# Kernel tuning notes

Hardware: AMD Instinct MI355X
Metric: run time of the kernel (lower is better)

Reference implementation:

```python
import jax, jax.numpy as jnp
import numpy as np

N = 8192        # num nodes == input_dim (attn is [N,N], indexed by edge endpoints)
E = 262144      # num edges (nnz of sparse G), avg degree 32
OD = 64         # output_dim


def setup_inputs() -> dict:
    key = jax.random.key(0)
    k_x, k_r, k_c, k_v, k_a, k_w = jax.random.split(key, 6)
    x = jax.random.normal(k_x, (N, N), dtype=jnp.float32)
    row = jax.random.randint(k_r, (E,), 0, N)
    col = jax.random.randint(k_c, (E,), 0, N)
    values = jax.random.uniform(k_v, (E,), dtype=jnp.float32)
    attn = jax.random.uniform(k_a, (N, N), dtype=jnp.float32)  # init uniform(0,1) per reset_parameters
    stdv = 1.0 / np.sqrt(OD)
    weight = jax.random.uniform(k_w, (N, OD), dtype=jnp.float32, minval=-stdv, maxval=stdv)
    return {"x": x, "attn": attn, "weight": weight, "values": values, "row": row, "col": col}


def reference(x, attn, weight, values, row, col):
    # x = x @ W : [N, OD]
    y = x @ weight
    # sparse_dense_mul: scale each edge's value by attn[row, col] (irregular gather)
    ev = values * attn[row, col]                      # [E]
    # torch.sparse.mm(G, y): out[i] = sum_{e: row[e]==i} ev[e] * y[col[e]]
    out = jax.ops.segment_sum(ev[:, None] * y[col], row, num_segments=x.shape[0])
    return (out, jnp.linalg.norm(attn))
```

## Files before the change

kernel.cpp:

```cpp
#include <hip/hip_runtime.h>
#include <hip/hip_bf16.h>

#define N 8192
#define OD 64
#define E_EDGES 262144

#define BM 64
#define BK 64
#define KSPLIT 16
#define KS_PER_SPLIT (N / KSPLIT)
#define NTILES (KS_PER_SPLIT / BK)
#define NORM_BLOCKS 2048
#define SCAT_BLOCKS 8192

typedef __attribute__((ext_vector_type(8))) short bf16x8;
typedef __attribute__((ext_vector_type(4))) float f32x4;

__device__ __forceinline__ unsigned short f2bf(float f) {
    union { float f; unsigned u; } v; v.f = f;
    unsigned r = (v.u + 0x7fffu + ((v.u >> 16) & 1u)) >> 16;
    return (unsigned short)r;
}

__device__ __forceinline__ void gload16(const void* g, void* l) {
    __builtin_amdgcn_global_load_lds(
        (const __attribute__((address_space(1))) unsigned int*)g,
        (__attribute__((address_space(3))) unsigned int*)l, 16, 0, 0);
}

__global__ __launch_bounds__(256) void prep_kernel(const float* __restrict__ attn,
                                                   const float* __restrict__ w,
                                                   unsigned short* __restrict__ wt,
                                                   float4* __restrict__ y4,
                                                   float4* __restrict__ out4,
                                                   float* __restrict__ part) {
    const int bid = blockIdx.x, t = threadIdx.x;

    if (t < 128) {
        int zi = bid * 128 + t;
        float4 z{0.f, 0.f, 0.f, 0.f};
        if (zi < 131072) y4[zi] = z;
        else out4[zi - 131072] = z;
    }

    if (bid < 128) {
        __shared__ unsigned short lds[64][80];
        const int kb = bid * 64;
        #pragma unroll
        for (int p = 0; p < 4; ++p) {
            int idx = p * 1024 + t * 4;
            int r = idx >> 6, c = idx & 63;
            float4 v = *(const float4*)(&w[(size_t)(kb + r) * OD + c]);
            lds[c + 0][r] = f2bf(v.x);
            lds[c + 1][r] = f2bf(v.y);
            lds[c + 2][r] = f2bf(v.z);
            lds[c + 3][r] = f2bf(v.w);
        }
        __syncthreads();
        const int colx = t >> 2, j0 = (t & 3) * 16;
        #pragma unroll
        for (int u = 0; u < 2; ++u) {
            *(bf16x8*)(wt + (size_t)colx * N + kb + j0 + u * 8) =
                *(const bf16x8*)(&lds[colx][j0 + u * 8]);
        }
    }

    const float4* a4 = (const float4*)attn;
    const int total = (N * (long)N) / 4;
    float s = 0.f;
    for (long i = (long)bid * 256 + t; i < total; i += (long)NORM_BLOCKS * 256) {
        float4 v = a4[i];
        s += v.x * v.x + v.y * v.y + v.z * v.z + v.w * v.w;
    }
    for (int off = 32; off > 0; off >>= 1) s += __shfl_down(s, off, 64);
    __shared__ float wpart[4];
    int wid = t >> 6;
    if ((t & 63) == 0) wpart[wid] = s;
    __syncthreads();
    if (t == 0) part[bid] = wpart[0] + wpart[1] + wpart[2] + wpart[3];
}

__global__ __launch_bounds__(256) void gemm_kernel(const float* __restrict__ x,
                                                   const unsigned short* __restrict__ wt,
                                                   float* __restrict__ y) {
    __shared__ float xs[2][BM * BK];
    __shared__ unsigned short bs[2][BM * BK];

    const int t = threadIdx.x;
    const int wv = t >> 6, lane = t & 63;
    const int lrow = lane & 15, g = lane >> 4;
    const int sw = lrow & 7;
    const int row0 = blockIdx.x * BM;
    const int k0 = blockIdx.y * KS_PER_SPLIT;

    const int xrow_b = t >> 4, xchunk = t & 15;
    const int brow_b = t >> 3, bchunk = t & 7;

    f32x4 acc[4] = {f32x4{0,0,0,0}, f32x4{0,0,0,0}, f32x4{0,0,0,0}, f32x4{0,0,0,0}};

    #define STAGE(buf, tile)                                                          \
        {                                                                             \
            const int kk = k0 + (tile) * BK;                                          \
            _Pragma("unroll")                                                         \
            for (int j = 0; j < 4; ++j) {                                             \
                int r = j * 16 + xrow_b;                                              \
                gload16(&x[(size_t)(row0 + r) * N + kk + ((xchunk ^ (r & 7)) << 2)],  \
                        &xs[buf][j * 1024 + t * 4]);                                  \
            }                                                                         \
            _Pragma("unroll")                                                         \
            for (int j = 0; j < 2; ++j) {                                             \
                int r = j * 32 + brow_b;                                              \
                gload16(&wt[(size_t)r * N + kk + ((bchunk ^ (r & 7)) << 3)],          \
                        &bs[buf][j * 2048 + t * 8]);                                  \
            }                                                                         \
        }

    STAGE(0, 0);
    asm volatile("s_waitcnt vmcnt(0)" ::: "memory");
    __syncthreads();

    int cur = 0;
    for (int tile = 0; tile < NTILES; ++tile) {
        if (tile + 1 < NTILES) STAGE(cur ^ 1, tile + 1);
        const int ar = wv * 16 + lrow;
        #pragma unroll
        for (int ks = 0; ks < 2; ++ks) {
            const int c0 = ks * 8 + g * 2;
            float4 lo = *(const float4*)&xs[cur][ar * 64 + ((c0 ^ sw) << 2)];
            float4 hi = *(const float4*)&xs[cur][ar * 64 + (((c0 + 1) ^ sw) << 2)];
            bf16x8 a;
            a[0] = f2bf(lo.x); a[1] = f2bf(lo.y); a[2] = f2bf(lo.z); a[3] = f2bf(lo.w);
            a[4] = f2bf(hi.x); a[5] = f2bf(hi.y); a[6] = f2bf(hi.z); a[7] = f2bf(hi.w);
            #pragma unroll
            for (int cf = 0; cf < 4; ++cf) {
                const int rb = cf * 16 + lrow;
                bf16x8 b = *(const bf16x8*)&bs[cur][rb * 64 + (((ks * 4 + g) ^ sw) << 3)];
                acc[cf] = __builtin_amdgcn_mfma_f32_16x16x32_bf16(a, b, acc[cf], 0, 0, 0);
            }
        }
        asm volatile("s_waitcnt vmcnt(0)" ::: "memory");
        __syncthreads();
        cur ^= 1;
    }

    float* yp = y + ((size_t)row0 + wv * 16 + g * 4) * OD;
    #pragma unroll
    for (int cf = 0; cf < 4; ++cf) {
        #pragma unroll
        for (int i = 0; i < 4; ++i)
            atomicAdd(&yp[i * OD + cf * 16 + lrow], acc[cf][i]);
    }
    #undef STAGE
}

__global__ __launch_bounds__(256) void scatter_kernel(const float* __restrict__ values,
                                                      const float* __restrict__ attn,
                                                      const int* __restrict__ row,
                                                      const int* __restrict__ col,
                                                      const float* __restrict__ y,
                                                      float* __restrict__ out,
                                                      const float* __restrict__ part,
                                                      float* __restrict__ out_norm) {
    if (blockIdx.x == SCAT_BLOCKS) {
        float s = 0.f;
        #pragma unroll
        for (int k = 0; k < NORM_BLOCKS / 256; ++k) s += part[k * 256 + threadIdx.x];
        for (int off = 32; off > 0; off >>= 1) s += __shfl_down(s, off, 64);
        __shared__ float wp[4];
        int wid = threadIdx.x >> 6;
        if ((threadIdx.x & 63) == 0) wp[wid] = s;
        __syncthreads();
        if (threadIdx.x == 0) *out_norm = sqrtf(wp[0] + wp[1] + wp[2] + wp[3]);
        return;
    }
    const int lane = threadIdx.x & 63;
    int e = blockIdx.x * 4 + (threadIdx.x >> 6);
    #pragma unroll
    for (int it = 0; it < E_EDGES / (SCAT_BLOCKS * 4); ++it, e += SCAT_BLOCKS * 4) {
        const int r = row[e];
        const int c = col[e];
        const float ev = values[e] * attn[(size_t)r * N + c];
        atomicAdd(&out[r * OD + lane], ev * y[c * OD + lane]);
    }
}

extern "C" void kernel_launch(void* const* d_in, const int* in_sizes, int n_in,
                              void* d_out, int out_size, void* d_ws, size_t ws_size,
                              hipStream_t stream) {
    const float* x      = (const float*)d_in[0];
    const float* attn   = (const float*)d_in[1];
    const float* weight = (const float*)d_in[2];
    const float* values = (const float*)d_in[3];
    const int*   row    = (const int*)d_in[4];
    const int*   col    = (const int*)d_in[5];
    float* out = (float*)d_out;

    char* wsb = (char*)d_ws;
    float*          part = (float*)wsb;
    unsigned short* wt   = (unsigned short*)(wsb + (1u << 20));
    float*          y    = (float*)(wsb + (2u << 20));

    prep_kernel<<<NORM_BLOCKS, 256, 0, stream>>>(attn, weight, wt, (float4*)y,
                                                 (float4*)out, part);
    gemm_kernel<<<dim3(N / BM, KSPLIT), 256, 0, stream>>>(x, wt, y);
    scatter_kernel<<<SCAT_BLOCKS + 1, 256, 0, stream>>>(values, attn, row, col, y, out,
                                                        part, out + (size_t)N * OD);
}
```

Before: 182.2 us.

## Move attn norm reduction into scatter kernel and batch edge loads

```diff
diff --git a/kernel.cpp b/kernel.cpp
--- a/kernel.cpp
+++ b/kernel.cpp
@@ -10,8 +10,8 @@
 #define KSPLIT 16
 #define KS_PER_SPLIT (N / KSPLIT)
 #define NTILES (KS_PER_SPLIT / BK)
-#define NORM_BLOCKS 2048
 #define SCAT_BLOCKS 8192
+#define EDGE_ITERS (E_EDGES / (SCAT_BLOCKS * 4))
 
 typedef __attribute__((ext_vector_type(8))) short bf16x8;
 typedef __attribute__((ext_vector_type(4))) float f32x4;
@@ -28,56 +28,37 @@
         (__attribute__((address_space(3))) unsigned int*)l, 16, 0, 0);
 }
 
-__global__ __launch_bounds__(256) void prep_kernel(const float* __restrict__ attn,
-                                                   const float* __restrict__ w,
+__global__ __launch_bounds__(256) void prep_kernel(const float* __restrict__ w,
                                                    unsigned short* __restrict__ wt,
                                                    float4* __restrict__ y4,
-                                                   float4* __restrict__ out4,
-                                                   float* __restrict__ part) {
+                                                   float4* __restrict__ out4) {
     const int bid = blockIdx.x, t = threadIdx.x;
-
-    if (t < 128) {
-        int zi = bid * 128 + t;
-        float4 z{0.f, 0.f, 0.f, 0.f};
-        if (zi < 131072) y4[zi] = z;
-        else out4[zi - 131072] = z;
-    }
-
-    if (bid < 128) {
-        __shared__ unsigned short lds[64][80];
-        const int kb = bid * 64;
-        #pragma unroll
-        for (int p = 0; p < 4; ++p) {
-            int idx = p * 1024 + t * 4;
-            int r = idx >> 6, c = idx & 63;
-            float4 v = *(const float4*)(&w[(size_t)(kb + r) * OD + c]);
-            lds[c + 0][r] = f2bf(v.x);
-            lds[c + 1][r] = f2bf(v.y);
-            lds[c + 2][r] = f2bf(v.z);
-            lds[c + 3][r] = f2bf(v.w);
-        }
-        __syncthreads();
-        const int colx = t >> 2, j0 = (t & 3) * 16;
-        #pragma unroll
-        for (int u = 0; u < 2; ++u) {
-            *(bf16x8*)(wt + (size_t)colx * N + kb + j0 + u * 8) =
-                *(const bf16x8*)(&lds[colx][j0 + u * 8]);
-        }
-    }
-
-    const float4* a4 = (const float4*)attn;
-    const int total = (N * (long)N) / 4;
-    float s = 0.f;
-    for (long i = (long)bid * 256 + t; i < total; i += (long)NORM_BLOCKS * 256) {
-        float4 v = a4[i];
-        s += v.x * v.x + v.y * v.y + v.z * v.z + v.w * v.w;
-    }
-    for (int off = 32; off > 0; off >>= 1) s += __shfl_down(s, off, 64);
-    __shared__ float wpart[4];
-    int wid = t >> 6;
-    if ((t & 63) == 0) wpart[wid] = s;
-    __syncthreads();
-    if (t == 0) part[bid] = wpart[0] + wpart[1] + wpart[2] + wpart[3];
+    const int base = bid * 256 + t;
+    float4 z{0.f, 0.f, 0.f, 0.f};
+    #pragma unroll
+    for (int u = 0; u < 4; ++u) y4[base + u * 32768] = z;
+    #pragma unroll
+    for (int u = 0; u < 4; ++u) out4[base + u * 32768] = z;
+
+    __shared__ unsigned short lds[64][80];
+    const int kb = bid * 64;
+    #pragma unroll
+    for (int p = 0; p < 4; ++p) {
+        int idx = p * 1024 + t * 4;
+        int r = idx >> 6, c = idx & 63;
+        float4 v = *(const float4*)(&w[(size_t)(kb + r) * OD + c]);
+        lds[c + 0][r] = f2bf(v.x);
+        lds[c + 1][r] = f2bf(v.y);
+        lds[c + 2][r] = f2bf(v.z);
+        lds[c + 3][r] = f2bf(v.w);
+    }
+    __syncthreads();
+    const int colx = t >> 2, j0 = (t & 3) * 16;
+    #pragma unroll
+    for (int u = 0; u < 2; ++u) {
+        *(bf16x8*)(wt + (size_t)colx * N + kb + j0 + u * 8) =
+            *(const bf16x8*)(&lds[colx][j0 + u * 8]);
+    }
 }
 
 __global__ __launch_bounds__(256) void gemm_kernel(const float* __restrict__ x,
@@ -153,35 +134,77 @@
     #undef STAGE
 }
 
-__global__ __launch_bounds__(256) void scatter_kernel(const float* __restrict__ values,
-                                                      const float* __restrict__ attn,
-                                                      const int* __restrict__ row,
-                                                      const int* __restrict__ col,
-                                                      const float* __restrict__ y,
-                                                      float* __restrict__ out,
-                                                      const float* __restrict__ part,
-                                                      float* __restrict__ out_norm) {
-    if (blockIdx.x == SCAT_BLOCKS) {
-        float s = 0.f;
-        #pragma unroll
-        for (int k = 0; k < NORM_BLOCKS / 256; ++k) s += part[k * 256 + threadIdx.x];
-        for (int off = 32; off > 0; off >>= 1) s += __shfl_down(s, off, 64);
-        __shared__ float wp[4];
-        int wid = threadIdx.x >> 6;
-        if ((threadIdx.x & 63) == 0) wp[wid] = s;
-        __syncthreads();
-        if (threadIdx.x == 0) *out_norm = sqrtf(wp[0] + wp[1] + wp[2] + wp[3]);
-        return;
-    }
-    const int lane = threadIdx.x & 63;
-    int e = blockIdx.x * 4 + (threadIdx.x >> 6);
-    #pragma unroll
-    for (int it = 0; it < E_EDGES / (SCAT_BLOCKS * 4); ++it, e += SCAT_BLOCKS * 4) {
-        const int r = row[e];
-        const int c = col[e];
-        const float ev = values[e] * attn[(size_t)r * N + c];
-        atomicAdd(&out[r * OD + lane], ev * y[c * OD + lane]);
-    }
+__device__ __forceinline__ void do_scatter(const float* __restrict__ values,
+                                           const float* __restrict__ attn,
+                                           const int* __restrict__ row,
+                                           const int* __restrict__ col,
+                                           const float* __restrict__ y,
+                                           float* __restrict__ out,
+                                           int bid, int t) {
+    const int lane = t & 63;
+    const int w = t >> 6;
+    int r8[EDGE_ITERS], c8[EDGE_ITERS];
+    float v8[EDGE_ITERS], a8[EDGE_ITERS];
+    #pragma unroll
+    for (int i = 0; i < EDGE_ITERS; ++i) {
+        int e = bid * 4 + w + i * (SCAT_BLOCKS * 4);
+        r8[i] = row[e]; c8[i] = col[e]; v8[i] = values[e];
+    }
+    #pragma unroll
+    for (int i = 0; i < EDGE_ITERS; ++i)
+        a8[i] = attn[(size_t)r8[i] * N + c8[i]];
+    #pragma unroll
+    for (int i = 0; i < EDGE_ITERS; ++i) {
+        float yv = y[c8[i] * OD + lane];
+        atomicAdd(&out[r8[i] * OD + lane], v8[i] * a8[i] * yv);
+    }
+}
+
+__device__ __forceinline__ float do_norm_part(const float* __restrict__ attn, int bid, int t) {
+    const float4* a4 = (const float4*)attn;
+    float s = 0.f;
+    int i = bid * 256 + t;
+    #pragma unroll
+    for (int u = 0; u < 8; ++u) {
+        float4 v = a4[i + u * (SCAT_BLOCKS * 256)];
+        s += v.x * v.x + v.y * v.y + v.z * v.z + v.w * v.w;
+    }
+    return s;
+}
+
+__global__ __launch_bounds__(256) void scatter_norm_kernel(
+        const float* __restrict__ values, const float* __restrict__ attn,
+        const int* __restrict__ row, const int* __restrict__ col,
+        const float* __restrict__ y, float* __restrict__ out,
+        float* __restrict__ part) {
+    const int bid = blockIdx.x, t = threadIdx.x;
+    float s;
+    if (bid & 1) {
+        s = do_norm_part(attn, bid, t);
+        do_scatter(values, attn, row, col, y, out, bid, t);
+    } else {
+        do_scatter(values, attn, row, col, y, out, bid, t);
+        s = do_norm_part(attn, bid, t);
+    }
+    for (int off = 32; off > 0; off >>= 1) s += __shfl_down(s, off, 64);
+    __shared__ float wpart[4];
+    int wid = t >> 6;
+    if ((t & 63) == 0) wpart[wid] = s;
+    __syncthreads();
+    if (t == 0) part[bid] = wpart[0] + wpart[1] + wpart[2] + wpart[3];
+}
+
+__global__ __launch_bounds__(256) void finalize_kernel(const float* __restrict__ part,
+                                                       float* __restrict__ out_norm) {
+    float s = 0.f;
+    #pragma unroll
+    for (int k = 0; k < SCAT_BLOCKS / 256; ++k) s += part[k * 256 + threadIdx.x];
+    for (int off = 32; off > 0; off >>= 1) s += __shfl_down(s, off, 64);
+    __shared__ float wp[4];
+    int wid = threadIdx.x >> 6;
+    if ((threadIdx.x & 63) == 0) wp[wid] = s;
+    __syncthreads();
+    if (threadIdx.x == 0) *out_norm = sqrtf(wp[0] + wp[1] + wp[2] + wp[3]);
 }
 
 extern "C" void kernel_launch(void* const* d_in, const int* in_sizes, int n_in,
@@ -200,9 +223,8 @@
     unsigned short* wt   = (unsigned short*)(wsb + (1u << 20));
     float*          y    = (float*)(wsb + (2u << 20));
 
-    prep_kernel<<<NORM_BLOCKS, 256, 0, stream>>>(attn, weight, wt, (float4*)y,
-                                                 (float4*)out, part);
+    prep_kernel<<<128, 256, 0, stream>>>(weight, wt, (float4*)y, (float4*)out);
     gemm_kernel<<<dim3(N / BM, KSPLIT), 256, 0, stream>>>(x, wt, y);
-    scatter_kernel<<<SCAT_BLOCKS + 1, 256, 0, stream>>>(values, attn, row, col, y, out,
-                                                        part, out + (size_t)N * OD);
-}
+    scatter_norm_kernel<<<SCAT_BLOCKS, 256, 0, stream>>>(values, attn, row, col, y, out, part);
+    finalize_kernel<<<1, 256, 0, stream>>>(part, out + (size_t)N * OD);
+}
```

New measurement: 164.7 us. -9.6%, faster.
